# Kernel tuning notes

Measured on AMD Instinct MI355X. Metric: run time of the kernel, lower is better.

The kernel has to match this reference:

```python
import jax, jax.numpy as jnp
import numpy as np

U, I, D, K, B, NNEG = 500000, 500000, 64, 32, 8192, 128
W1, W2, W3, W4 = 1e-6, 1.0, 1e-6, 1.0
NEG_WEIGHT, GAMMA, LAMBDA = 200.0, 1e-4, 2.5


def setup_inputs() -> dict:
    key = jax.random.key(0)
    ks = jax.random.split(key, 14)
    return {
        "users": jax.random.randint(ks[0], (B,), 0, U),
        "pos_items": jax.random.randint(ks[1], (B,), 0, I),
        "neg_items": jax.random.randint(ks[2], (B, NNEG), 0, I),
        "rpkms": jax.random.normal(ks[3], (B,), dtype=jnp.float32),
        "user_emb": jax.random.normal(ks[4], (U, D), dtype=jnp.float32) * 1e-2,
        "item_emb": jax.random.normal(ks[5], (I, D), dtype=jnp.float32) * 1e-2,
        "beta_uD": jax.random.uniform(ks[6], (U,), dtype=jnp.float32),
        "beta_iD": jax.random.uniform(ks[7], (I,), dtype=jnp.float32),
        "ii_neighbor_mat": jax.random.randint(ks[8], (I, K), 0, I),
        "ii_constraint_mat": jax.random.uniform(ks[9], (I, K), dtype=jnp.float32),
        "mse_u_w": jax.random.normal(ks[10], (D, D), dtype=jnp.float32) * 0.05,
        "mse_u_b": jnp.zeros((D,), jnp.float32),
        "mse_i_w": jax.random.normal(ks[11], (D, D), dtype=jnp.float32) * 0.05,
        "mse_i_b": jnp.zeros((D,), jnp.float32),
        "fc1_w1": jax.random.normal(ks[12], (D, 2 * D), dtype=jnp.float32) * 0.05,
        "fc1_b1": jnp.zeros((D,), jnp.float32),
        "fc1_w2": jax.random.normal(ks[13], (1, D), dtype=jnp.float32) * 0.05,
        "fc1_b2": jnp.zeros((1,), jnp.float32),
    }


def reference(users, pos_items, neg_items, rpkms, user_emb, item_emb,
              beta_uD, beta_iD, ii_neighbor_mat, ii_constraint_mat,
              mse_u_w, mse_u_b, mse_i_w, mse_i_b,
              fc1_w1, fc1_b1, fc1_w2, fc1_b2):
    sp = jax.nn.softplus  # -log(sigmoid(x)) == softplus(-x)

    ue = user_emb[users]            # [B, D]
    pe = item_emb[pos_items]        # [B, D]
    ne = item_emb[neg_items]        # [B, N, D]

    # ---- omegas ----
    pos_w = W1 + W2 * beta_uD[users] * beta_iD[pos_items]          # [B]
    neg_w = W3 + W4 * beta_uD[users][:, None] * beta_iD[neg_items]  # [B, N]

    # ---- cal_loss_L (weighted BCE with logits) ----
    pos_scores = jnp.sum(ue * pe, axis=-1)                  # [B]
    neg_scores = jnp.einsum('bd,bnd->bn', ue, ne)           # [B, N]
    pos_loss = pos_w * sp(-pos_scores)                      # label 1
    neg_loss = jnp.mean(neg_w * sp(neg_scores), axis=-1)    # label 0, mean over negs
    loss_L = jnp.mean(pos_loss + neg_loss * NEG_WEIGHT)

    # ---- norm_loss over all learned parameters ----
    params = (user_emb, item_emb, mse_u_w, mse_u_b, mse_i_w, mse_i_b,
              fc1_w1, fc1_b1, fc1_w2, fc1_b2)
    norm = GAMMA * 0.5 * sum(jnp.sum(p * p) for p in params)

    # ---- cal_loss_I: gather item-item neighbors of pos_items ----
    nbr = item_emb[ii_neighbor_mat[pos_items]]              # [B, K, D]
    sim = ii_constraint_mat[pos_items]                      # [B, K]
    loss_I = LAMBDA * jnp.mean(sim * sp(-jnp.einsum('bd,bkd->bk', ue, nbr)))

    # ---- mse_loss ----
    feat_u = ue @ mse_u_w.T + mse_u_b
    feat_i = pe @ mse_i_w.T + mse_i_b
    pred = jnp.sum(feat_u * feat_i, axis=-1)
    mse = jnp.mean((pred - rpkms) ** 2)

    total = loss_L + norm + loss_I + mse
    zero = jnp.float32(0.0)  # torch returns torch.tensor(0.0) as 4th element
    return jnp.stack([total, loss_L, loss_I, zero, mse, norm])
```

## Files before the change

### kernel.cpp

```cpp
#include <hip/hip_runtime.h>
#include <math.h>

#define UU 500000
#define II 500000
#define DD 64
#define KK 32
#define BB 8192
#define NNEG 128

typedef float v4f __attribute__((ext_vector_type(4)));
typedef float v2f __attribute__((ext_vector_type(2)));

__device__ __forceinline__ float softplus_f(float x) {
    return fmaxf(x, 0.0f) + log1pf(expf(-fabsf(x)));
}

__device__ __forceinline__ float waveReduceSum(float v) {
#pragma unroll
    for (int off = 32; off > 0; off >>= 1) v += __shfl_xor(v, off, 64);
    return v;
}

__global__ __launch_bounds__(256) void norm_convert_kernel(
    const float* __restrict__ user_emb, const float* __restrict__ item_emb,
    unsigned int* __restrict__ f8it,
    const float* __restrict__ mse_u_w, const float* __restrict__ mse_u_b,
    const float* __restrict__ mse_i_w, const float* __restrict__ mse_i_b,
    const float* __restrict__ fc1_w1, const float* __restrict__ fc1_b1,
    const float* __restrict__ fc1_w2, const float* __restrict__ fc1_b2,
    float* __restrict__ acc)
{
    const size_t tid = (size_t)blockIdx.x * blockDim.x + threadIdx.x;
    const size_t st  = (size_t)gridDim.x * blockDim.x;
    float s = 0.f;

    {
        const size_t n16 = (size_t)II * DD / 16;
        const v4f* it4 = (const v4f*)item_emb;
        uint4* out4 = (uint4*)f8it;
        for (size_t k = tid; k < n16; k += st) {
            v4f a = __builtin_nontemporal_load(&it4[4 * k]);
            v4f b = __builtin_nontemporal_load(&it4[4 * k + 1]);
            v4f c = __builtin_nontemporal_load(&it4[4 * k + 2]);
            v4f d = __builtin_nontemporal_load(&it4[4 * k + 3]);
            s += a.x*a.x + a.y*a.y + a.z*a.z + a.w*a.w;
            s += b.x*b.x + b.y*b.y + b.z*b.z + b.w*b.w;
            s += c.x*c.x + c.y*c.y + c.z*c.z + c.w*c.w;
            s += d.x*d.x + d.y*d.y + d.z*d.z + d.w*d.w;
            uint4 w;
            w.x = __builtin_amdgcn_cvt_pk_fp8_f32(a.x * 64.f, a.y * 64.f, 0u,  false);
            w.x = __builtin_amdgcn_cvt_pk_fp8_f32(a.z * 64.f, a.w * 64.f, w.x, true);
            w.y = __builtin_amdgcn_cvt_pk_fp8_f32(b.x * 64.f, b.y * 64.f, 0u,  false);
            w.y = __builtin_amdgcn_cvt_pk_fp8_f32(b.z * 64.f, b.w * 64.f, w.y, true);
            w.z = __builtin_amdgcn_cvt_pk_fp8_f32(c.x * 64.f, c.y * 64.f, 0u,  false);
            w.z = __builtin_amdgcn_cvt_pk_fp8_f32(c.z * 64.f, c.w * 64.f, w.z, true);
            w.w = __builtin_amdgcn_cvt_pk_fp8_f32(d.x * 64.f, d.y * 64.f, 0u,  false);
            w.w = __builtin_amdgcn_cvt_pk_fp8_f32(d.z * 64.f, d.w * 64.f, w.w, true);
            out4[k] = w;
        }
    }
    {
        const size_t n4 = (size_t)UU * DD / 4;
        const v4f* a = (const v4f*)user_emb;
        for (size_t i = tid; i < n4; i += st) {
            v4f x = __builtin_nontemporal_load(&a[i]);
            s += x.x*x.x + x.y*x.y + x.z*x.z + x.w*x.w;
        }
    }
    for (size_t i = tid; i < (size_t)DD * DD; i += st)
        s += mse_u_w[i] * mse_u_w[i] + mse_i_w[i] * mse_i_w[i];
    for (size_t i = tid; i < (size_t)DD * 2 * DD; i += st)
        s += fc1_w1[i] * fc1_w1[i];
    for (size_t i = tid; i < (size_t)DD; i += st)
        s += mse_u_b[i] * mse_u_b[i] + mse_i_b[i] * mse_i_b[i]
           + fc1_b1[i] * fc1_b1[i] + fc1_w2[i] * fc1_w2[i];
    if (tid == 0) s += fc1_b2[0] * fc1_b2[0];

    s = waveReduceSum(s);
    __shared__ float red[4];
    if ((threadIdx.x & 63) == 0) red[threadIdx.x >> 6] = s;
    __syncthreads();
    if (threadIdx.x == 0)
        atomicAdd(&acc[2], red[0] + red[1] + red[2] + red[3]);
}

__global__ __launch_bounds__(256) void gather_mse_kernel(
    const int* __restrict__ users, const int* __restrict__ pos_items,
    const int* __restrict__ neg_items, const float* __restrict__ rpkms,
    const float* __restrict__ user_emb, const float* __restrict__ item_emb,
    const unsigned int* __restrict__ f8it,
    const float* __restrict__ beta_uD, const float* __restrict__ beta_iD,
    const int* __restrict__ ii_nbr, const float* __restrict__ ii_con,
    const float* __restrict__ mse_u_w, const float* __restrict__ mse_u_b,
    const float* __restrict__ mse_i_w, const float* __restrict__ mse_i_b,
    float* __restrict__ acc, unsigned int* __restrict__ cnt,
    float* __restrict__ out)
{
    const int wave = threadIdx.x >> 6;
    const int lane = threadIdx.x & 63;
    const int b = blockIdx.x * 4 + wave;

    const int u_idx = users[b];
    const int p_idx = pos_items[b];
    const float u_reg = user_emb[(size_t)u_idx * DD + lane];
    const float p_reg = item_emb[(size_t)p_idx * DD + lane];
    const float bu = beta_uD[u_idx];

    __shared__ float sU[4][DD];
    __shared__ float sP[4][DD];
    sU[wave][lane] = u_reg;
    sP[wave][lane] = p_reg;

    const int q  = lane & 3;
    const int li = lane >> 2;

    float4 uv[4];
#pragma unroll
    for (int j = 0; j < 4; ++j)
        uv[j] = *(const float4*)&sU[wave][q * 16 + j * 4];

    float accL = 0.f, accI = 0.f, accM = 0.f;

    {
        const float pos_dot = waveReduceSum(u_reg * p_reg);
        if (lane == 0)
            accL += (1e-6f + bu * beta_iD[p_idx]) * softplus_f(-pos_dot);
    }

    const int i0 = neg_items[(size_t)b * NNEG + lane];
    const int i1 = neg_items[(size_t)b * NNEG + 64 + lane];
    const float bn0 = beta_iD[i0];
    const float bn1 = beta_iD[i1];
    int nbv = 0; float simv = 0.f;
    if (lane < KK) {
        nbv  = ii_nbr[(size_t)p_idx * KK + lane];
        simv = ii_con[(size_t)p_idx * KK + lane];
    }

    const float negscale4 = 0.25f * (200.0f / (float)NNEG);
    const float inv64 = 0.015625f;

    uint4 rg[4];
    float rw[4];

#define PREP(g, slot)                                                          \
    {                                                                          \
        int idx; float w;                                                      \
        if ((g) < 4)      { idx = __shfl(i0, (g) * 16 + li, 64);               \
                            w   = __shfl(bn0, (g) * 16 + li, 64); }            \
        else if ((g) < 8) { idx = __shfl(i1, ((g) - 4) * 16 + li, 64);         \
                            w   = __shfl(bn1, ((g) - 4) * 16 + li, 64); }      \
        else              { idx = __shfl(nbv, ((g) - 8) * 16 + li, 64);        \
                            w   = __shfl(simv, ((g) - 8) * 16 + li, 64); }     \
        rg[slot] = ((const uint4*)(f8it + (size_t)idx * (DD / 4)))[q];         \
        rw[slot] = w;                                                          \
    }

#define DOT4(u32, vv, d)                                                       \
    {                                                                          \
        v2f lo = __builtin_amdgcn_cvt_pk_f32_fp8((u32), false);                \
        v2f hi = __builtin_amdgcn_cvt_pk_f32_fp8((u32), true);                 \
        d = fmaf(lo.x, (vv).x, d); d = fmaf(lo.y, (vv).y, d);                  \
        d = fmaf(hi.x, (vv).z, d); d = fmaf(hi.y, (vv).w, d);                  \
    }

#define CONSUME(g, slot)                                                       \
    {                                                                          \
        float dot = 0.f;                                                       \
        DOT4(rg[slot].x, uv[0], dot);                                          \
        DOT4(rg[slot].y, uv[1], dot);                                          \
        DOT4(rg[slot].z, uv[2], dot);                                          \
        DOT4(rg[slot].w, uv[3], dot);                                          \
        dot *= inv64;                                                          \
        dot += __shfl_xor(dot, 1, 64);                                         \
        dot += __shfl_xor(dot, 2, 64);                                         \
        if ((g) < 8) accL += negscale4 * (1e-6f + bu * rw[slot]) * softplus_f(dot); \
        else         accI += 0.25f * rw[slot] * softplus_f(-dot);              \
    }

    PREP(0, 0); PREP(1, 1); PREP(2, 2); PREP(3, 3);
    CONSUME(0, 0); PREP(4, 0);
    CONSUME(1, 1); PREP(5, 1);
    CONSUME(2, 2); PREP(6, 2);
    CONSUME(3, 3); PREP(7, 3);
    CONSUME(4, 0); PREP(8, 0);
    CONSUME(5, 1); PREP(9, 1);
    CONSUME(6, 2);
    CONSUME(7, 3);
    CONSUME(8, 0);
    CONSUME(9, 1);
#undef PREP
#undef DOT4
#undef CONSUME

    {
        float4 pv[4];
#pragma unroll
        for (int j = 0; j < 4; ++j)
            pv[j] = *(const float4*)&sP[wave][q * 16 + j * 4];
        float pq = 0.f;
#pragma unroll
        for (int g = 0; g < 4; ++g) {
            const int r = g * 16 + li;
            const float* wur = mse_u_w + r * DD + q * 16;
            const float* wir = mse_i_w + r * DD + q * 16;
            float fu = 0.f, fi = 0.f;
#pragma unroll
            for (int j = 0; j < 4; ++j) {
                const float4 a = *(const float4*)(wur + j * 4);
                fu = fmaf(a.x, uv[j].x, fu); fu = fmaf(a.y, uv[j].y, fu);
                fu = fmaf(a.z, uv[j].z, fu); fu = fmaf(a.w, uv[j].w, fu);
                const float4 c = *(const float4*)(wir + j * 4);
                fi = fmaf(c.x, pv[j].x, fi); fi = fmaf(c.y, pv[j].y, fi);
                fi = fmaf(c.z, pv[j].z, fi); fi = fmaf(c.w, pv[j].w, fi);
            }
            fu += __shfl_xor(fu, 1, 64); fu += __shfl_xor(fu, 2, 64);
            fi += __shfl_xor(fi, 1, 64); fi += __shfl_xor(fi, 2, 64);
            fu += mse_u_b[r];
            fi += mse_i_b[r];
            pq += fu * fi;
        }
        const float pred = waveReduceSum(pq) * 0.25f;
        if (lane == 0) {
            const float diff = pred - rpkms[b];
            accM += diff * diff;
        }
    }

    accL = waveReduceSum(accL);
    accI = waveReduceSum(accI);
    __shared__ float redL[4], redI[4], redM[4];
    if (lane == 0) { redL[wave] = accL; redI[wave] = accI; redM[wave] = accM; }
    __syncthreads();
    if (threadIdx.x == 0) {
        atomicAdd(&acc[0], redL[0] + redL[1] + redL[2] + redL[3]);
        atomicAdd(&acc[1], redI[0] + redI[1] + redI[2] + redI[3]);
        atomicAdd(&acc[3], redM[0] + redM[1] + redM[2] + redM[3]);
        __threadfence();
        const unsigned int t = atomicAdd(cnt, 1u);
        if (t == (unsigned int)(gridDim.x - 1)) {
            const float sL  = atomicAdd(&acc[0], 0.0f);
            const float sI  = atomicAdd(&acc[1], 0.0f);
            const float sNo = atomicAdd(&acc[2], 0.0f);
            const float sM  = atomicAdd(&acc[3], 0.0f);
            const float loss_L = sL / (float)BB;
            const float loss_I = 2.5f * sI / (float)(BB * KK);
            const float mse    = sM / (float)BB;
            const float nrm    = 1e-4f * 0.5f * sNo;
            out[0] = loss_L + nrm + loss_I + mse;
            out[1] = loss_L;
            out[2] = loss_I;
            out[3] = 0.0f;
            out[4] = mse;
            out[5] = nrm;
        }
    }
}

#define NORMB 1024
__global__ __launch_bounds__(256) void fb_fused_kernel(
    const int* __restrict__ users, const int* __restrict__ pos_items,
    const int* __restrict__ neg_items,
    const float* __restrict__ user_emb, const float* __restrict__ item_emb,
    const float* __restrict__ beta_uD, const float* __restrict__ beta_iD,
    const int* __restrict__ ii_nbr, const float* __restrict__ ii_con,
    const float* __restrict__ mse_u_w, const float* __restrict__ mse_u_b,
    const float* __restrict__ mse_i_w, const float* __restrict__ mse_i_b,
    const float* __restrict__ fc1_w1, const float* __restrict__ fc1_b1,
    const float* __restrict__ fc1_w2, const float* __restrict__ fc1_b2,
    float* __restrict__ acc)
{
    const int wave = threadIdx.x >> 6;
    const int lane = threadIdx.x & 63;
    __shared__ float red[4];

    if (blockIdx.x < NORMB) {
        const size_t tid = (size_t)blockIdx.x * blockDim.x + threadIdx.x;
        const size_t st  = (size_t)NORMB * 256;
        const size_t n4  = (size_t)UU * DD / 4;
        float s = 0.f;
        const v4f* a = (const v4f*)user_emb;
        for (size_t i = tid; i < n4; i += st) {
            v4f x = a[i]; s += x.x*x.x + x.y*x.y + x.z*x.z + x.w*x.w;
        }
        const v4f* c = (const v4f*)item_emb;
        for (size_t i = tid; i < n4; i += st) {
            v4f x = c[i]; s += x.x*x.x + x.y*x.y + x.z*x.z + x.w*x.w;
        }
        for (size_t i = tid; i < (size_t)DD * DD; i += st)
            s += mse_u_w[i] * mse_u_w[i] + mse_i_w[i] * mse_i_w[i];
        for (size_t i = tid; i < (size_t)DD * 2 * DD; i += st)
            s += fc1_w1[i] * fc1_w1[i];
        for (size_t i = tid; i < (size_t)DD; i += st)
            s += mse_u_b[i] * mse_u_b[i] + mse_i_b[i] * mse_i_b[i]
               + fc1_b1[i] * fc1_b1[i] + fc1_w2[i] * fc1_w2[i];
        if (tid == 0) s += fc1_b2[0] * fc1_b2[0];
        s = waveReduceSum(s);
        if (lane == 0) red[wave] = s;
        __syncthreads();
        if (threadIdx.x == 0)
            atomicAdd(&acc[2], red[0] + red[1] + red[2] + red[3]);
        return;
    }

    const int b = (blockIdx.x - NORMB) * 4 + wave;
    float accL = 0.f, accI = 0.f;
    const int u_idx = users[b];
    const int p_idx = pos_items[b];
    const float u_reg = user_emb[(size_t)u_idx * DD + lane];
    const float bu = beta_uD[u_idx];
    __shared__ float sU[4][DD];
    sU[wave][lane] = u_reg;
    const int q  = lane & 3;
    const int li = lane >> 2;
    float4 uv[4];
#pragma unroll
    for (int j = 0; j < 4; ++j) uv[j] = *(const float4*)&sU[wave][j * 16 + q * 4];
    {
        const float p = item_emb[(size_t)p_idx * DD + lane];
        const float pos_dot = waveReduceSum(u_reg * p);
        if (lane == 0) accL += (1e-6f + bu * beta_iD[p_idx]) * softplus_f(-pos_dot);
    }
    const int i0 = neg_items[(size_t)b * NNEG + lane];
    const int i1 = neg_items[(size_t)b * NNEG + 64 + lane];
    const float bn0 = beta_iD[i0];
    const float bn1 = beta_iD[i1];
    const float negscale4 = 0.25f * (200.0f / (float)NNEG);
#pragma unroll
    for (int g = 0; g < 2; ++g) {
        const int   srcI = g ? i1 : i0;
        const float srcB = g ? bn1 : bn0;
        float4 vb[4][4]; float bi4[4];
#pragma unroll
        for (int t = 0; t < 4; ++t) {
            const int n = t * 16 + li;
            const int idx = __shfl(srcI, n, 64);
            bi4[t] = __shfl(srcB, n, 64);
            const float* row = item_emb + (size_t)idx * DD + q * 4;
#pragma unroll
            for (int j = 0; j < 4; ++j) vb[t][j] = *(const float4*)(row + j * 16);
        }
#pragma unroll
        for (int t = 0; t < 4; ++t) {
            float dot = 0.f;
#pragma unroll
            for (int j = 0; j < 4; ++j) {
                dot = fmaf(vb[t][j].x, uv[j].x, dot);
                dot = fmaf(vb[t][j].y, uv[j].y, dot);
                dot = fmaf(vb[t][j].z, uv[j].z, dot);
                dot = fmaf(vb[t][j].w, uv[j].w, dot);
            }
            dot += __shfl_xor(dot, 1, 64);
            dot += __shfl_xor(dot, 2, 64);
            accL += negscale4 * (1e-6f + bu * bi4[t]) * softplus_f(dot);
        }
    }
    int nbv = 0; float simv = 0.f;
    if (lane < KK) {
        nbv  = ii_nbr[(size_t)p_idx * KK + lane];
        simv = ii_con[(size_t)p_idx * KK + lane];
    }
    {
        float4 vb[2][4]; float sk2[2];
#pragma unroll
        for (int t = 0; t < 2; ++t) {
            const int n = t * 16 + li;
            const int idx = __shfl(nbv, n, 64);
            sk2[t] = __shfl(simv, n, 64);
            const float* row = item_emb + (size_t)idx * DD + q * 4;
#pragma unroll
            for (int j = 0; j < 4; ++j) vb[t][j] = *(const float4*)(row + j * 16);
        }
#pragma unroll
        for (int t = 0; t < 2; ++t) {
            float dot = 0.f;
#pragma unroll
            for (int j = 0; j < 4; ++j) {
                dot = fmaf(vb[t][j].x, uv[j].x, dot);
                dot = fmaf(vb[t][j].y, uv[j].y, dot);
                dot = fmaf(vb[t][j].z, uv[j].z, dot);
                dot = fmaf(vb[t][j].w, uv[j].w, dot);
            }
            dot += __shfl_xor(dot, 1, 64);
            dot += __shfl_xor(dot, 2, 64);
            accI += 0.25f * sk2[t] * softplus_f(-dot);
        }
    }
    accL = waveReduceSum(accL);
    accI = waveReduceSum(accI);
    __shared__ float redL[4], redI[4];
    if (lane == 0) { redL[wave] = accL; redI[wave] = accI; }
    __syncthreads();
    if (threadIdx.x == 0) {
        atomicAdd(&acc[0], redL[0] + redL[1] + redL[2] + redL[3]);
        atomicAdd(&acc[1], redI[0] + redI[1] + redI[2] + redI[3]);
    }
}

__global__ __launch_bounds__(256) void fb_mse_kernel(
    const int* __restrict__ users, const int* __restrict__ pos_items,
    const float* __restrict__ rpkms,
    const float* __restrict__ user_emb, const float* __restrict__ item_emb,
    const float* __restrict__ mse_u_w, const float* __restrict__ mse_u_b,
    const float* __restrict__ mse_i_w, const float* __restrict__ mse_i_b,
    float* __restrict__ acc)
{
    __shared__ float sWu[DD * (DD + 1)];
    __shared__ float sWi[DD * (DD + 1)];
    __shared__ float sBu[DD], sBi[DD];
    __shared__ float sUe[4][DD], sPe[4][DD];
    for (int i = threadIdx.x; i < DD * DD; i += blockDim.x) {
        const int r = i >> 6, c = i & 63;
        sWu[r * (DD + 1) + c] = mse_u_w[i];
        sWi[r * (DD + 1) + c] = mse_i_w[i];
    }
    if (threadIdx.x < DD) {
        sBu[threadIdx.x] = mse_u_b[threadIdx.x];
        sBi[threadIdx.x] = mse_i_b[threadIdx.x];
    }
    const int wave = threadIdx.x >> 6;
    const int lane = threadIdx.x & 63;
    const int b = blockIdx.x * 4 + wave;
    sUe[wave][lane] = user_emb[(size_t)users[b] * DD + lane];
    sPe[wave][lane] = item_emb[(size_t)pos_items[b] * DD + lane];
    __syncthreads();
    float fu = sBu[lane];
    float fi = sBi[lane];
#pragma unroll 8
    for (int d = 0; d < DD; ++d) {
        fu += sUe[wave][d] * sWu[lane * (DD + 1) + d];
        fi += sPe[wave][d] * sWi[lane * (DD + 1) + d];
    }
    const float pred = waveReduceSum(fu * fi);
    if (lane == 0) {
        const float diff = pred - rpkms[b];
        atomicAdd(&acc[3], diff * diff);
    }
}

__global__ void finalize_kernel(const float* __restrict__ acc, float* __restrict__ out)
{
    if (threadIdx.x == 0) {
        const float loss_L = acc[0] / (float)BB;
        const float loss_I = 2.5f * acc[1] / (float)(BB * KK);
        const float mse    = acc[3] / (float)BB;
        const float norm   = 1e-4f * 0.5f * acc[2];
        const float total  = loss_L + norm + loss_I + mse;
        out[0] = total;
        out[1] = loss_L;
        out[2] = loss_I;
        out[3] = 0.0f;
        out[4] = mse;
        out[5] = norm;
    }
}

extern "C" void kernel_launch(void* const* d_in, const int* in_sizes, int n_in,
                              void* d_out, int out_size, void* d_ws, size_t ws_size,
                              hipStream_t stream)
{
    const int*   users      = (const int*)  d_in[0];
    const int*   pos_items  = (const int*)  d_in[1];
    const int*   neg_items  = (const int*)  d_in[2];
    const float* rpkms      = (const float*)d_in[3];
    const float* user_emb   = (const float*)d_in[4];
    const float* item_emb   = (const float*)d_in[5];
    const float* beta_uD    = (const float*)d_in[6];
    const float* beta_iD    = (const float*)d_in[7];
    const int*   ii_nbr     = (const int*)  d_in[8];
    const float* ii_con     = (const float*)d_in[9];
    const float* mse_u_w    = (const float*)d_in[10];
    const float* mse_u_b    = (const float*)d_in[11];
    const float* mse_i_w    = (const float*)d_in[12];
    const float* mse_i_b    = (const float*)d_in[13];
    const float* fc1_w1     = (const float*)d_in[14];
    const float* fc1_b1     = (const float*)d_in[15];
    const float* fc1_w2     = (const float*)d_in[16];
    const float* fc1_b2     = (const float*)d_in[17];

    float* acc = (float*)d_ws;
    unsigned int* cnt = (unsigned int*)d_ws + 4;
    hipMemsetAsync(d_ws, 0, 8 * sizeof(float), stream);

    const size_t f8_bytes = (size_t)II * DD;
    const size_t need = 256 + f8_bytes;

    if (ws_size >= need) {
        unsigned int* f8it = (unsigned int*)((char*)d_ws + 256);
        norm_convert_kernel<<<4096, 256, 0, stream>>>(
            user_emb, item_emb, f8it,
            mse_u_w, mse_u_b, mse_i_w, mse_i_b,
            fc1_w1, fc1_b1, fc1_w2, fc1_b2, acc);
        gather_mse_kernel<<<BB / 4, 256, 0, stream>>>(
            users, pos_items, neg_items, rpkms,
            user_emb, item_emb, f8it, beta_uD, beta_iD,
            ii_nbr, ii_con, mse_u_w, mse_u_b, mse_i_w, mse_i_b,
            acc, cnt, (float*)d_out);
    } else {
        fb_fused_kernel<<<NORMB + BB / 4, 256, 0, stream>>>(
            users, pos_items, neg_items,
            user_emb, item_emb, beta_uD, beta_iD, ii_nbr, ii_con,
            mse_u_w, mse_u_b, mse_i_w, mse_i_b,
            fc1_w1, fc1_b1, fc1_w2, fc1_b2, acc);
        fb_mse_kernel<<<BB / 4, 256, 0, stream>>>(
            users, pos_items, rpkms, user_emb, item_emb,
            mse_u_w, mse_u_b, mse_i_w, mse_i_b, acc);
        finalize_kernel<<<1, 64, 0, stream>>>(acc, (float*)d_out);
    }
}
```

Measured before the change: 504.1 us.

## Convert item table last at finer granularity and add cache-warming pass before gather

```diff
diff --git a/kernel.cpp b/kernel.cpp
--- a/kernel.cpp
+++ b/kernel.cpp
@@ -35,31 +35,6 @@
     float s = 0.f;
 
     {
-        const size_t n16 = (size_t)II * DD / 16;
-        const v4f* it4 = (const v4f*)item_emb;
-        uint4* out4 = (uint4*)f8it;
-        for (size_t k = tid; k < n16; k += st) {
-            v4f a = __builtin_nontemporal_load(&it4[4 * k]);
-            v4f b = __builtin_nontemporal_load(&it4[4 * k + 1]);
-            v4f c = __builtin_nontemporal_load(&it4[4 * k + 2]);
-            v4f d = __builtin_nontemporal_load(&it4[4 * k + 3]);
-            s += a.x*a.x + a.y*a.y + a.z*a.z + a.w*a.w;
-            s += b.x*b.x + b.y*b.y + b.z*b.z + b.w*b.w;
-            s += c.x*c.x + c.y*c.y + c.z*c.z + c.w*c.w;
-            s += d.x*d.x + d.y*d.y + d.z*d.z + d.w*d.w;
-            uint4 w;
-            w.x = __builtin_amdgcn_cvt_pk_fp8_f32(a.x * 64.f, a.y * 64.f, 0u,  false);
-            w.x = __builtin_amdgcn_cvt_pk_fp8_f32(a.z * 64.f, a.w * 64.f, w.x, true);
-            w.y = __builtin_amdgcn_cvt_pk_fp8_f32(b.x * 64.f, b.y * 64.f, 0u,  false);
-            w.y = __builtin_amdgcn_cvt_pk_fp8_f32(b.z * 64.f, b.w * 64.f, w.y, true);
-            w.z = __builtin_amdgcn_cvt_pk_fp8_f32(c.x * 64.f, c.y * 64.f, 0u,  false);
-            w.z = __builtin_amdgcn_cvt_pk_fp8_f32(c.z * 64.f, c.w * 64.f, w.z, true);
-            w.w = __builtin_amdgcn_cvt_pk_fp8_f32(d.x * 64.f, d.y * 64.f, 0u,  false);
-            w.w = __builtin_amdgcn_cvt_pk_fp8_f32(d.z * 64.f, d.w * 64.f, w.w, true);
-            out4[k] = w;
-        }
-    }
-    {
         const size_t n4 = (size_t)UU * DD / 4;
         const v4f* a = (const v4f*)user_emb;
         for (size_t i = tid; i < n4; i += st) {
@@ -76,12 +51,45 @@
            + fc1_b1[i] * fc1_b1[i] + fc1_w2[i] * fc1_w2[i];
     if (tid == 0) s += fc1_b2[0] * fc1_b2[0];
 
+    {
+        const size_t npair = (size_t)II * DD / 8;
+        const v4f* it4 = (const v4f*)item_emb;
+        uint2* out2 = (uint2*)f8it;
+        for (size_t k = tid; k < npair; k += st) {
+            v4f a = __builtin_nontemporal_load(&it4[2 * k]);
+            v4f b = __builtin_nontemporal_load(&it4[2 * k + 1]);
+            s += a.x*a.x + a.y*a.y + a.z*a.z + a.w*a.w;
+            s += b.x*b.x + b.y*b.y + b.z*b.z + b.w*b.w;
+            uint2 w;
+            w.x = __builtin_amdgcn_cvt_pk_fp8_f32(a.x * 64.f, a.y * 64.f, 0u,  false);
+            w.x = __builtin_amdgcn_cvt_pk_fp8_f32(a.z * 64.f, a.w * 64.f, w.x, true);
+            w.y = __builtin_amdgcn_cvt_pk_fp8_f32(b.x * 64.f, b.y * 64.f, 0u,  false);
+            w.y = __builtin_amdgcn_cvt_pk_fp8_f32(b.z * 64.f, b.w * 64.f, w.y, true);
+            out2[k] = w;
+        }
+    }
+
     s = waveReduceSum(s);
     __shared__ float red[4];
     if ((threadIdx.x & 63) == 0) red[threadIdx.x >> 6] = s;
     __syncthreads();
     if (threadIdx.x == 0)
         atomicAdd(&acc[2], red[0] + red[1] + red[2] + red[3]);
+}
+
+__global__ __launch_bounds__(256) void warm_table_kernel(
+    const unsigned int* __restrict__ f8it)
+{
+    const size_t tid = (size_t)blockIdx.x * blockDim.x + threadIdx.x;
+    const size_t st  = (size_t)gridDim.x * blockDim.x;
+    const size_t n4  = (size_t)II * DD / 16;
+    const uint4* t4 = (const uint4*)f8it;
+    unsigned int s = 0;
+    for (size_t i = tid; i < n4; i += st) {
+        uint4 x = t4[i];
+        s ^= x.x ^ x.y ^ x.z ^ x.w;
+    }
+    asm volatile("" :: "v"(s));
 }
 
 __global__ __launch_bounds__(256) void gather_mse_kernel(
@@ -491,6 +499,7 @@
             user_emb, item_emb, f8it,
             mse_u_w, mse_u_b, mse_i_w, mse_i_b,
             fc1_w1, fc1_b1, fc1_w2, fc1_b2, acc);
+        warm_table_kernel<<<2048, 256, 0, stream>>>(f8it);
         gather_mse_kernel<<<BB / 4, 256, 0, stream>>>(
             users, pos_items, neg_items, rpkms,
             user_emb, item_emb, f8it, beta_uD, beta_iD,
```

Result: no change. 504.3 us (+0.0%).
